# Optimization experiments

Measured on AMD Instinct MI355X. Metric: run time of the kernel, lower is better.

## Reference

```python
import jax, jax.numpy as jnp
import numpy as np

NUM_LABELS = 1000


def setup_inputs() -> dict:
    key = jax.random.key(0)
    k1, k2 = jax.random.split(key)
    outputs = jax.random.normal(k1, (64, 512, NUM_LABELS), dtype=jnp.float32)
    labels = jax.random.randint(k2, (64, 512), 0, NUM_LABELS, dtype=jnp.int32)
    return {"outputs": outputs, "labels": labels}


def reference(outputs, labels):
    L = outputs.shape[-1]
    flat = outputs.reshape(-1, L)        # [N, L]
    labs = labels.reshape(-1)            # [N]

    # State: index_selection [L] (the permutation torch derives via
    # argmax(encode_transfer, 1)) and unswitched-label membership mask [L].
    # torch.inner(ET, eye[select_col]) permutes ET's COLUMNS by select_col
    # (a transposition), which composes onto index_selection as
    # new_idx = select_col[old_idx].
    def step(carry, xs):
        idx_sel, unsw = carry
        y, lab = xs
        r = jnp.argmax(y[idx_sel]).astype(idx_sel.dtype)  # switched argmax
        lab_unsw = unsw[lab]
        do_swap = (r != lab) & lab_unsw
        # apply transposition (r <-> lab) to idx_sel when do_swap
        swapped = jnp.where(idx_sel == r, lab,
                            jnp.where(idx_sel == lab, r, idx_sel))
        new_idx = jnp.where(do_swap, swapped, idx_sel)
        # label is removed from unswitched set whenever it was a member
        # (both the mismatch-swap branch and the match branch remove it)
        new_unsw = unsw.at[lab].set(False)
        return (new_idx, new_unsw), None

    init = (jnp.arange(L, dtype=jnp.int32), jnp.ones((L,), dtype=bool))
    (idx_final, _), _ = jax.lax.scan(step, init, (flat, labs))

    # torch returns index_select on the flattened outputs with the FINAL
    # index_selection
    return jnp.take(flat, idx_final, axis=-1)
```

## Files before the change

kernel.cpp:

```cpp
#include <hip/hip_runtime.h>
#include <climits>
#include <cstdint>

#define L 1000
#define NROWS 32768


__global__ void k_init(int* __restrict__ first_row) {
    int i = blockIdx.x * blockDim.x + threadIdx.x;
    if (i < L) first_row[i] = INT_MAX;
}

__global__ void k_first(const int* __restrict__ labels, int* __restrict__ first_row) {
    int i = blockIdx.x * blockDim.x + threadIdx.x;
    if (i < NROWS) atomicMin(&first_row[labels[i]], i);
}

__global__ void k_argmax(const float* __restrict__ flat, const int* __restrict__ first_row,
                         int* __restrict__ evt_g) {
    int lab = blockIdx.x;
    int row = first_row[lab];
    if (row >= NROWS) return;
    const float* y = flat + (size_t)row * L;
    int tid = threadIdx.x;
    float bv = -INFINITY;
    int bk = 0x7fffffff;
    for (int k = tid; k < L; k += 256) {
        float v = y[k];
        if (v > bv) { bv = v; bk = k; }
    }
    int cnt = 0;
    for (int j = tid; j < L; j += 256) cnt += (first_row[j] < row) ? 1 : 0;
    __shared__ float sv[256];
    __shared__ int   sk[256];
    __shared__ int   sc[256];
    sv[tid] = bv; sk[tid] = bk; sc[tid] = cnt;
    __syncthreads();
    for (int off = 128; off > 0; off >>= 1) {
        if (tid < off) {
            float v2 = sv[tid + off]; int k2 = sk[tid + off];
            if (v2 > sv[tid] || (v2 == sv[tid] && k2 < sk[tid])) { sv[tid] = v2; sk[tid] = k2; }
            sc[tid] += sc[tid + off];
        }
        __syncthreads();
    }
    if (tid == 0) evt_g[sc[0]] = (lab << 10) | sk[0];
}

__global__ void __launch_bounds__(1024) k_seq(const int* __restrict__ first_row,
                                              const int* __restrict__ evt_g,
                                              int* __restrict__ perm_g) {
    __shared__ int evt[1008];
    __shared__ int pos[L];
    int tid = threadIdx.x;
    int present = (tid < L) && (first_row[tid] < NROWS);
    int K = __syncthreads_count(present);
    if (tid < K) evt[tid] = evt_g[tid];
    if (tid >= K && tid < K + 4) evt[tid] = 0;
    if (tid < L) pos[tid] = tid;
    __syncthreads();
    if (tid == 0 && K > 0) {
        int e0 = evt[0], e1 = evt[1];
        int e2 = evt[2], e3 = evt[3];
        int r    = e0 & 1023, lab = e0 >> 10;
        int Plab = lab;
        int pr   = r;
        int m1 = e1 & 1023, l1 = e1 >> 10;
        int Pm1 = m1, Pl1 = l1;
        for (int i = 0; i < K; i++) {
            pos[r]   = Plab;
            pos[lab] = pr;
            int rn  = (m1 == r) ? Plab : (m1 == lab) ? pr : Pm1;
            int prn = pos[rn];
            int Pln = (l1 == r) ? Plab : (l1 == lab) ? pr : Pl1;
            int m2 = e2 & 1023, l2 = e2 >> 10;
            int Pm2 = pos[m2];
            int Pl2 = pos[l2];
            int e4  = evt[i + 4];
            r = rn; lab = l1; Plab = Pln; pr = prn;
            m1 = m2; l1 = l2; Pm1 = Pm2; Pl1 = Pl2;
            e2 = e3; e3 = e4;
        }
    }
    __syncthreads();
    if (tid < L) perm_g[pos[tid]] = tid;
}

__global__ void __launch_bounds__(1024) k_gather(const float* __restrict__ flat,
                                                 const int* __restrict__ perm_g,
                                                 float* __restrict__ out) {
    __shared__ __align__(16) int   p[1024];
    __shared__ __align__(16) float buf[4][L];
    int tid = threadIdx.x;
    if (tid < L) p[tid] = perm_g[tid];
    int g = tid >> 8;
    int t = tid & 255;
    size_t row = (size_t)blockIdx.x * 4 + g;
    const float* src = flat + row * L;
    float*       dst = out  + row * L;
    float4 v;
    if (t < 250) v = ((const float4*)src)[t];
    __syncthreads();
    if (t < 250) ((float4*)buf[g])[t] = v;
    __syncthreads();
    if (t < 250) {
        int j = t * 4;
        float4 o;
        o.x = buf[g][p[j + 0]];
        o.y = buf[g][p[j + 1]];
        o.z = buf[g][p[j + 2]];
        o.w = buf[g][p[j + 3]];
        ((float4*)dst)[t] = o;
    }
}

extern "C" void kernel_launch(void* const* d_in, const int* in_sizes, int n_in,
                              void* d_out, int out_size, void* d_ws, size_t ws_size,
                              hipStream_t stream) {
    const float* flat   = (const float*)d_in[0];
    const int*   labels = (const int*)d_in[1];
    float* out = (float*)d_out;
    int* ws = (int*)d_ws;
    int* first_row = ws;
    int* evt_g     = ws + 1024;
    int* perm_g    = ws + 2048;

    k_init  <<<(L + 255) / 256, 256, 0, stream>>>(first_row);
    k_first <<<(NROWS + 255) / 256, 256, 0, stream>>>(labels, first_row);
    k_argmax<<<L, 256, 0, stream>>>(flat, first_row, evt_g);
    k_seq   <<<1, 1024, 0, stream>>>(first_row, evt_g, perm_g);
    k_gather<<<NROWS / 4, 1024, 0, stream>>>(flat, perm_g, out);
}
```

Baseline: 307.6 us.

## Deepen software pipeline of serial permutation loop with delayed writes and forwarding

Restructures the single-thread sequential swap loop in k_seq so that shared-memory loads for events are issued two iterations ahead and the second write of each transposition is deferred by one iteration, with register forwarding resolving address conflicts. The goal is to take LDS load latency off the loop-carried dependency chain, which dominates this serial step. It adds comparison logic and dummy scratch slots (pos enlarged to 1024, extra evt padding), and the forwarding logic is error-prone.

```diff
diff --git a/kernel.cpp b/kernel.cpp
--- a/kernel.cpp
+++ b/kernel.cpp
@@ -51,36 +51,52 @@
                                               const int* __restrict__ evt_g,
                                               int* __restrict__ perm_g) {
     __shared__ int evt[1008];
-    __shared__ int pos[L];
+    __shared__ int pos[1024];
     int tid = threadIdx.x;
     int present = (tid < L) && (first_row[tid] < NROWS);
     int K = __syncthreads_count(present);
     if (tid < K) evt[tid] = evt_g[tid];
-    if (tid >= K && tid < K + 4) evt[tid] = 0;
+    if (tid >= K && tid < K + 7) evt[tid] = 0;
     if (tid < L) pos[tid] = tid;
     __syncthreads();
     if (tid == 0 && K > 0) {
-        int e0 = evt[0], e1 = evt[1];
-        int e2 = evt[2], e3 = evt[3];
-        int r    = e0 & 1023, lab = e0 >> 10;
-        int Plab = lab;
-        int pr   = r;
-        int m1 = e1 & 1023, l1 = e1 >> 10;
-        int Pm1 = m1, Pl1 = l1;
+        int e0 = evt[0], e1 = evt[1], e2 = evt[2];
+        int r0 = e0 & 1023, l0 = e0 >> 10;
+        int Pl0 = l0, praw = r0;
+        int rq = 1017, lq = 1016, Plq = 0;
+        int lqq = 1018, Mprev = 0, praw_q = 0;
+        int m1 = e1 & 1023, l1 = e1 >> 10, a1 = m1, b1 = l1;
+        int m2 = e2 & 1023, l2 = e2 >> 10, a2 = m2, b2 = l2;
+        int w3 = evt[3], w4 = evt[4];
         for (int i = 0; i < K; i++) {
-            pos[r]   = Plab;
-            pos[lab] = pr;
-            int rn  = (m1 == r) ? Plab : (m1 == lab) ? pr : Pm1;
-            int prn = pos[rn];
-            int Pln = (l1 == r) ? Plab : (l1 == lab) ? pr : Pl1;
-            int m2 = e2 & 1023, l2 = e2 >> 10;
-            int Pm2 = pos[m2];
-            int Pl2 = pos[l2];
-            int e4  = evt[i + 4];
-            r = rn; lab = l1; Plab = Pln; pr = prn;
-            m1 = m2; l1 = l2; Pm1 = Pm2; Pl1 = Pl2;
-            e2 = e3; e3 = e4;
+            pos[r0] = Pl0;
+            int Mcur = (rq == lqq) ? Mprev : praw_q;
+            int waddr = (lq == r0) ? 1016 : lq;
+            pos[waddr] = Mcur;
+            int m3 = w3 & 1023, l3 = w3 >> 10;
+            int a3 = pos[m3];
+            int b3 = pos[l3];
+            int r1f = (m1 == lqq) ? Mprev : a1;
+            r1f = (m1 == rq) ? Plq : r1f;
+            r1f = (m1 == lq) ? Mcur : r1f;
+            r1f = (m1 == r0) ? Pl0 : r1f;
+            if (m1 == l0) {
+                asm volatile("" ::: "memory");
+                r1f = (r0 == lq) ? Mcur : praw;
+            }
+            int Pl1f = (l1 == rq) ? Plq : b1;
+            Pl1f = (l1 == r0) ? Pl0 : Pl1f;
+            int prawn = pos[r1f];
+            int wn = evt[i + 5];
+            Mprev = Mcur; praw_q = praw;
+            lqq = lq; rq = r0; Plq = Pl0; lq = l0;
+            r0 = r1f; l0 = l1; Pl0 = Pl1f; praw = prawn;
+            m1 = m2; l1 = l2; a1 = a2; b1 = b2;
+            m2 = m3; l2 = l3; a2 = a3; b2 = b3;
+            w3 = w4; w4 = wn;
         }
+        int Mfin = (rq == lqq) ? Mprev : praw_q;
+        pos[lq] = Mfin;
     }
     __syncthreads();
     if (tid < L) perm_g[pos[tid]] = tid;
```

Result: slower. 425.0 us (+38.2%).
